# Kernel optimization log

Measured on AMD Instinct MI355X. Metric: run time of the kernel, lower is better.

## Reference

```python
import jax, jax.numpy as jnp
import numpy as np

T = 2048        # Tmax encoder frames
EPROJS = 1024   # encoder projection dim (Henc)
DUNITS = 512    # prediction net hidden
EMBED = 512     # embedding dim
JOINT = 512     # joint space dim
ODIM = 10000    # output vocab
BLANK = 0


def setup_inputs() -> dict:
    key = jax.random.key(0)
    ks = jax.random.split(key, 11)
    def g(k, shape, scale):
        return (jax.random.normal(k, shape, dtype=jnp.float32) * scale)
    inp = {
        'h': jax.random.normal(ks[0], (T, EPROJS), dtype=jnp.float32),
        # Embedding with padding_idx=blank -> blank row zeroed
        'embed': g(ks[1], (ODIM, EMBED), 0.05).at[BLANK].set(0.0),
        # LSTMCell params (torch gate order: i, f, g, o)
        'W_ih': g(ks[2], (4 * DUNITS, EMBED), 1.0 / np.sqrt(EMBED)),
        'W_hh': g(ks[3], (4 * DUNITS, DUNITS), 1.0 / np.sqrt(DUNITS)),
        'b_ih': g(ks[4], (4 * DUNITS,), 0.01),
        'b_hh': g(ks[5], (4 * DUNITS,), 0.01),
        # joint network
        'W_enc': g(ks[6], (JOINT, EPROJS), 1.0 / np.sqrt(EPROJS)),
        'b_enc': g(ks[7], (JOINT,), 0.01),
        'W_dec': g(ks[8], (JOINT, DUNITS), 1.0 / np.sqrt(DUNITS)),  # no bias
        'W_out': g(ks[9], (ODIM, JOINT), 1.0 / np.sqrt(JOINT)),
        'b_out': g(ks[10], (ODIM,), 0.01),
    }
    return inp


def _lstm_cell(x, h_prev, c_prev, W_ih, W_hh, b_ih, b_hh):
    gates = W_ih @ x + b_ih + W_hh @ h_prev + b_hh  # (4*DUNITS,)
    i, f, g, o = jnp.split(gates, 4)
    c = jax.nn.sigmoid(f) * c_prev + jax.nn.sigmoid(i) * jnp.tanh(g)
    h = jax.nn.sigmoid(o) * jnp.tanh(c)
    return h, c


def reference(h, embed, W_ih, W_hh, b_ih, b_hh, W_enc, b_enc, W_dec, W_out, b_out):
    # Precompute encoder-side joint projection (same math, hoisted out of loop)
    h_proj = h @ W_enc.T + b_enc  # (T, JOINT)

    # Initial prediction-net step on zero embedding from zero state
    zeros_e = jnp.zeros((EMBED,), dtype=h.dtype)
    zeros_d = jnp.zeros((DUNITS,), dtype=h.dtype)
    y0, c0 = _lstm_cell(zeros_e, zeros_d, zeros_d, W_ih, W_hh, b_ih, b_hh)

    def step(carry, hp_t):
        y, c, score = carry
        # joint: tanh(lin_enc(h_t) + lin_dec(y)) -> lin_out -> log_softmax
        ytu = jax.nn.log_softmax(W_out @ jnp.tanh(hp_t + W_dec @ y) + b_out)
        logp = jnp.max(ytu)
        pred = jnp.argmax(ytu)
        emitted = pred != BLANK
        # Candidate prediction-net update with embedded token
        ey = embed[pred]
        y_new, c_new = _lstm_cell(ey, y, c, W_ih, W_hh, b_ih, b_hh)
        y = jnp.where(emitted, y_new, y)
        c = jnp.where(emitted, c_new, c)
        score = score + jnp.where(emitted, logp, jnp.zeros_like(logp))
        tok = jnp.where(emitted, pred, BLANK).astype(jnp.int32)
        return (y, c, score), tok

    (y, c, score), yseq = jax.lax.scan(step, (y0, c0, jnp.float32(0.0)), h_proj)
    # yseq: (T,) int32, BLANK where no symbol was emitted at that frame
    return yseq, score
```

## Files before the change

kernel.cpp:

```cpp
#include <hip/hip_runtime.h>
#include <stdint.h>

typedef unsigned long long u64;
typedef uint32_t u32;

#define NB     256
#define NT     256
#define TMAX   2048
#define EPROJS 1024
#define DUNITS 512
#define EMBED  512
#define JOINT  512
#define ODIM   10000

#define N_LSTM 32
#define DEC0   32
#define CONS0  48
#define N_CONS 208
#define MAGIC  0xD07ED07Eu

#define WS_YB   0
#define WS_UD   4096
#define WS_PK   8192
#define WS_SA   10240
#define WS_DN   12288
#define WS_HP   16384

__device__ __forceinline__ float aloadf(const float* p){
  return __hip_atomic_load(p, __ATOMIC_RELAXED, __HIP_MEMORY_SCOPE_AGENT);
}
__device__ __forceinline__ void astoref(float* p, float v){
  __hip_atomic_store(p, v, __ATOMIC_RELAXED, __HIP_MEMORY_SCOPE_AGENT);
}
__device__ __forceinline__ u64 aloadu64(const u64* p){
  return __hip_atomic_load(p, __ATOMIC_RELAXED, __HIP_MEMORY_SCOPE_AGENT);
}
__device__ __forceinline__ void astoreu64(u64* p, u64 v){
  __hip_atomic_store(p, v, __ATOMIC_RELAXED, __HIP_MEMORY_SCOPE_AGENT);
}
__device__ __forceinline__ u32 aloadu32(const u32* p){
  return __hip_atomic_load(p, __ATOMIC_RELAXED, __HIP_MEMORY_SCOPE_AGENT);
}
__device__ __forceinline__ void astoreu32(u32* p, u32 v){
  __hip_atomic_store(p, v, __ATOMIC_RELAXED, __HIP_MEMORY_SCOPE_AGENT);
}

__device__ __forceinline__ u32 ordbits(float f){
  u32 u = __float_as_uint(f);
  return (u & 0x80000000u) ? ~u : (u | 0x80000000u);
}
__device__ __forceinline__ float unordbits(u32 o){
  u32 u = (o & 0x80000000u) ? (o & 0x7fffffffu) : ~o;
  return __uint_as_float(u);
}
__device__ __forceinline__ float sigmoidf_(float x){ return 1.0f/(1.0f+expf(-x)); }

__device__ __forceinline__ float wredsum(float v){
  #pragma unroll
  for (int o=32;o>0;o>>=1) v += __shfl_xor(v, o);
  return v;
}
__device__ __forceinline__ u64 wredmax64(u64 v){
  #pragma unroll
  for (int o=32;o>0;o>>=1){ u64 x = __shfl_xor(v, o); v = (x>v)?x:v; }
  return v;
}

#define LOAD8(dst, baseptr) { const float4* _p=(const float4*)(baseptr); \
  float4 _a=_p[0], _b=_p[1]; \
  dst[0]=_a.x; dst[1]=_a.y; dst[2]=_a.z; dst[3]=_a.w; \
  dst[4]=_b.x; dst[5]=_b.y; dst[6]=_b.z; dst[7]=_b.w; }

#define LDS8(dst, base) { float4 _a=*(const float4*)(base); \
  float4 _b=*(const float4*)((base)+4); \
  dst[0]=_a.x; dst[1]=_a.y; dst[2]=_a.z; dst[3]=_a.w; \
  dst[4]=_b.x; dst[5]=_b.y; dst[6]=_b.z; dst[7]=_b.w; }

__global__ void rnnt_init(char* ws){
  u32* p = (u32*)ws;
  for (int i = threadIdx.x; i < 4096; i += blockDim.x) p[i] = 0u;
}

__global__ void __launch_bounds__(NT, 1)
rnnt_decode(const float* __restrict__ h,    const float* __restrict__ embed,
            const float* __restrict__ W_ih, const float* __restrict__ W_hh,
            const float* __restrict__ b_ih, const float* __restrict__ b_hh,
            const float* __restrict__ W_enc,const float* __restrict__ b_enc,
            const float* __restrict__ W_dec,const float* __restrict__ W_out,
            const float* __restrict__ b_out,
            float* __restrict__ out, char* __restrict__ ws)
{
  const int b    = blockIdx.x;
  const int tid  = threadIdx.x;
  const int lane = tid & 63;
  const int w    = tid >> 6;

  u64*   ybuf = (u64*)(ws + WS_YB);
  u64*   udec = (u64*)(ws + WS_UD);
  u64*   packs= (u64*)(ws + WS_PK);
  u64*   sarr = (u64*)(ws + WS_SA);
  u32*   done = (u32*)(ws + WS_DN);
  float* hp   = (float*)(ws + WS_HP);

  __shared__ float smem[8192];
  float* PL = smem;
  float* EL = &smem[4416];
  float* YL = &smem[4928];
  float* ZL = &smem[5440];
  float* GL = &smem[5952];
  u64*   R64= (u64*)&smem[6016];
  float* RF = &smem[6024];

  {
    float (*lds_h)[EPROJS] = (float(*)[EPROJS])smem;
    #pragma unroll
    for (int r=0;r<8;r++){
      const float4 hv = *(const float4*)(h + (size_t)(8*b + r)*EPROJS + tid*4);
      *(float4*)&lds_h[r][tid*4] = hv;
    }
    __syncthreads();
    for (int p=0;p<2;p++){
      const int j = p*NT + tid;
      float acc[8] = {0,0,0,0,0,0,0,0};
      const float4* wrow = (const float4*)(W_enc + (size_t)j*EPROJS);
      for (int k4=0;k4<EPROJS/4;k4++){
        const float4 wv = wrow[k4];
        #pragma unroll
        for (int t8=0;t8<8;t8++){
          const float4 hv = *(const float4*)&lds_h[t8][k4*4];
          acc[t8] = fmaf(wv.x,hv.x, fmaf(wv.y,hv.y, fmaf(wv.z,hv.z, fmaf(wv.w,hv.w, acc[t8]))));
        }
      }
      const float be = b_enc[j];
      #pragma unroll
      for (int t8=0;t8<8;t8++)
        astoref(&hp[(size_t)(8*b+t8)*JOINT + j], acc[t8] + be);
    }
    asm volatile("s_waitcnt vmcnt(0)" ::: "memory");
    if (tid==0) astoreu32(&done[b], MAGIC);
    __syncthreads();
  }

  if (b < N_LSTM){
    const int d = b;
    float wih[16][8], whh[16][8];
    #pragma unroll
    for (int q=0;q<16;q++){
      const int gr = w*DUNITS + 16*d + q;
      LOAD8(wih[q], W_ih + (size_t)gr*EMBED  + lane*8);
      LOAD8(whh[q], W_hh + (size_t)gr*DUNITS + lane*8);
    }
    float bias_r = 0.0f;
    if (tid < 64){
      const int gr = (tid>>4)*DUNITS + 16*d + (tid&15);
      bias_r = b_ih[gr] + b_hh[gr];
    }
    float c_st = 0.0f, y_st = 0.0f;
    if (tid < 16){
      const int j = 16*d + tid;
      const float gi = b_ih[j]            + b_hh[j];
      const float gg = b_ih[2*DUNITS + j] + b_hh[2*DUNITS + j];
      const float go = b_ih[3*DUNITS + j] + b_hh[3*DUNITS + j];
      c_st = sigmoidf_(gi)*tanhf(gg);
      y_st = sigmoidf_(go)*tanhf(c_st);
      astoreu64(&ybuf[j], ((u64)1u<<32) | (u64)__float_as_uint(y_st));
    }

    for (int t=0;t<TMAX;t++){
      const u32 tg = (u32)(t+1);
      u64 ya, yb;
      for(;;){
        ya = aloadu64(&ybuf[2*tid]); yb = aloadu64(&ybuf[2*tid+1]);
        const int ok = ((u32)(ya>>32)==tg) & ((u32)(yb>>32)==tg);
        if (__syncthreads_and(ok)) break;
      }
      YL[2*tid]   = __uint_as_float((u32)ya);
      YL[2*tid+1] = __uint_as_float((u32)yb);
      __syncthreads();
      float y8[8]; LDS8(y8, &YL[8*lane]);
      float vp[16];
      #pragma unroll
      for (int q=0;q<16;q++){
        float a=0.f;
        #pragma unroll
        for (int k=0;k<8;k++) a = fmaf(whh[q][k], y8[k], a);
        vp[q] = a;
      }
      u64 pk = 0;
      for(;;){
        if (tid < N_CONS) pk = aloadu64(&packs[tid]);
        const int ok = (tid < N_CONS) ? ((u32)(pk>>48)==tg) : 1;
        if (__syncthreads_and(ok)) break;
      }
      { u64 m = wredmax64(pk); if (lane==0) R64[w]=m; }
      __syncthreads();
      if (tid==0){
        u64 bb=R64[0];
        #pragma unroll
        for (int i=1;i<4;i++) bb = (R64[i]>bb)?R64[i]:bb;
        R64[0]=bb;
      }
      __syncthreads();
      const u64 best = R64[0];
      const int pred = (int)((~(u32)best) & 0xFFFFu);
      const int emitted = (pred != 0);
      __syncthreads();
      const float2 ev = *(const float2*)(embed + (size_t)pred*EMBED + 2*tid);
      EL[2*tid] = ev.x; EL[2*tid+1] = ev.y;
      __syncthreads();
      float e8[8]; LDS8(e8, &EL[8*lane]);
      #pragma unroll
      for (int q=0;q<16;q++){
        float a = vp[q];
        #pragma unroll
        for (int k=0;k<8;k++) a = fmaf(wih[q][k], e8[k], a);
        PL[(w*16+q)*68 + lane] = a;
      }
      __syncthreads();
      if (tid < 64){
        const float* row = &PL[tid*68];
        float s = bias_r;
        #pragma unroll
        for (int k4=0;k4<16;k4++){
          const float4 v4 = *(const float4*)&row[4*k4];
          s += v4.x + v4.y + v4.z + v4.w;
        }
        GL[tid] = s;
      }
      __syncthreads();
      if (tid < 16){
        const float gi=GL[tid], gf=GL[16+tid], gg=GL[32+tid], go=GL[48+tid];
        const float cn = sigmoidf_(gf)*c_st + sigmoidf_(gi)*tanhf(gg);
        const float yn = sigmoidf_(go)*tanhf(cn);
        if (emitted){ c_st = cn; y_st = yn; }
        astoreu64(&ybuf[16*d + tid], ((u64)(tg+1)<<32) | (u64)__float_as_uint(y_st));
      }
    }
  }
  else if (b < CONS0){
    const int dd = b - DEC0;
    float wdec[8][8];
    #pragma unroll
    for (int q=0;q<8;q++){
      const int r = 32*dd + 8*w + q;
      LOAD8(wdec[q], W_dec + (size_t)r*DUNITS + lane*8);
    }
    for (int t=0;t<TMAX;t++){
      const u32 tg = (u32)(t+1);
      u64 ya, yb;
      for(;;){
        ya = aloadu64(&ybuf[2*tid]); yb = aloadu64(&ybuf[2*tid+1]);
        const int ok = ((u32)(ya>>32)==tg) & ((u32)(yb>>32)==tg);
        if (__syncthreads_and(ok)) break;
      }
      YL[2*tid]   = __uint_as_float((u32)ya);
      YL[2*tid+1] = __uint_as_float((u32)yb);
      __syncthreads();
      float y8[8]; LDS8(y8, &YL[8*lane]);
      #pragma unroll
      for (int q=0;q<8;q++){
        float a=0.f;
        #pragma unroll
        for (int k=0;k<8;k++) a = fmaf(wdec[q][k], y8[k], a);
        PL[(8*w+q)*68 + lane] = a;
      }
      __syncthreads();
      if (tid < 32){
        const float* row = &PL[tid*68];
        float s = 0.f;
        #pragma unroll
        for (int k4=0;k4<16;k4++){
          const float4 v4 = *(const float4*)&row[4*k4];
          s += v4.x + v4.y + v4.z + v4.w;
        }
        astoreu64(&udec[32*dd + tid], ((u64)tg<<32) | (u64)__float_as_uint(s));
      }
      __syncthreads();
    }
  }
  else {
    const int cb = b - CONS0;
    const int rowstart = (cb<16) ? cb*49 : 784 + (cb-16)*48;
    const int rowcnt   = (cb<16) ? 49 : 48;
    float wout[13][8];
    #pragma unroll
    for (int q=0;q<13;q++){
      const int s = 13*w + q;
      if (s < rowcnt){
        LOAD8(wout[q], W_out + (size_t)(rowstart+s)*JOINT + lane*8);
      } else {
        #pragma unroll
        for (int k=0;k<8;k++) wout[q][k]=0.f;
      }
    }
    float my_bo = 0.f; int my_row = 0; bool my_val = false;
    if (tid < rowcnt){ my_val = true; my_row = rowstart + tid; my_bo = b_out[my_row]; }

    for(;;){
      const int ok = (aloadu32(&done[tid]) == MAGIC);
      if (__syncthreads_and(ok)) break;
    }

    float score = 0.0f;
    for (int t=0;t<TMAX;t++){
      const u32 tg = (u32)(t+1);
      u64 ua, ub;
      for(;;){
        ua = aloadu64(&udec[2*tid]); ub = aloadu64(&udec[2*tid+1]);
        const int ok = ((u32)(ua>>32)==tg) & ((u32)(ub>>32)==tg);
        if (__syncthreads_and(ok)) break;
      }
      const float u0 = __uint_as_float((u32)ua);
      const float u1 = __uint_as_float((u32)ub);
      const float h0 = aloadf(&hp[(size_t)t*JOINT + 2*tid]);
      const float h1 = aloadf(&hp[(size_t)t*JOINT + 2*tid + 1]);
      ZL[2*tid]   = tanhf(h0 + u0);
      ZL[2*tid+1] = tanhf(h1 + u1);
      __syncthreads();
      float z8[8]; LDS8(z8, &ZL[8*lane]);
      #pragma unroll
      for (int q=0;q<13;q++){
        float a=0.f;
        #pragma unroll
        for (int k=0;k<8;k++) a = fmaf(wout[q][k], z8[k], a);
        PL[(13*w+q)*68 + lane] = a;
      }
      __syncthreads();
      u64 key = 0; float lg = 0.f;
      if (tid < 52){
        const float* row = &PL[tid*68];
        float s = my_bo;
        #pragma unroll
        for (int k4=0;k4<16;k4++){
          const float4 v4 = *(const float4*)&row[4*k4];
          s += v4.x + v4.y + v4.z + v4.w;
        }
        lg = s;
        if (my_val) key = ((u64)ordbits(lg)<<16) | (u64)(0xFFFFu & ~(u32)my_row);
      }
      if (w == 0){
        const u64 bk = wredmax64(key);
        const float mw = unordbits((u32)(bk>>16));
        const float e  = my_val ? __expf(lg - mw) : 0.f;
        const float sw = wredsum(e);
        if (lane == 0){
          astoreu64(&sarr[cb],  ((u64)tg<<32) | (u64)__float_as_uint(sw));
          astoreu64(&packs[cb], ((u64)tg<<48) | bk);
        }
      }
      if (b == CONS0){
        u64 pk = 0, sa = 0;
        for(;;){
          if (tid < N_CONS){ pk = aloadu64(&packs[tid]); sa = aloadu64(&sarr[tid]); }
          const int ok = (tid < N_CONS) ?
            (((u32)(pk>>48)==tg) & ((u32)(sa>>32)==tg)) : 1;
          if (__syncthreads_and(ok)) break;
        }
        { u64 m = wredmax64(pk); if (lane==0) R64[w]=m; }
        __syncthreads();
        if (tid==0){
          u64 bb=R64[0];
          #pragma unroll
          for (int i=1;i<4;i++) bb = (R64[i]>bb)?R64[i]:bb;
          R64[0]=bb;
        }
        __syncthreads();
        const u64 best = R64[0];
        const float mstar = unordbits((u32)(best>>16));
        float term = (tid < N_CONS) ?
          __uint_as_float((u32)sa) * __expf(unordbits((u32)(pk>>16)) - mstar) : 0.f;
        term = wredsum(term);
        if (lane==0) RF[w]=term;
        __syncthreads();
        if (tid==0){
          const float S = RF[0]+RF[1]+RF[2]+RF[3];
          const int pred = (int)((~(u32)best) & 0xFFFFu);
          if (pred != 0) score += -logf(S);
          out[t] = (float)pred;
        }
        __syncthreads();
      } else {
        __syncthreads();
      }
    }
    if (b == CONS0 && tid == 0) out[TMAX] = score;
  }
}

extern "C" void kernel_launch(void* const* d_in, const int* in_sizes, int n_in,
                              void* d_out, int out_size, void* d_ws, size_t ws_size,
                              hipStream_t stream)
{
  const float* h     = (const float*)d_in[0];
  const float* embed = (const float*)d_in[1];
  const float* W_ih  = (const float*)d_in[2];
  const float* W_hh  = (const float*)d_in[3];
  const float* b_ih  = (const float*)d_in[4];
  const float* b_hh  = (const float*)d_in[5];
  const float* W_enc = (const float*)d_in[6];
  const float* b_enc = (const float*)d_in[7];
  const float* W_dec = (const float*)d_in[8];
  const float* W_out = (const float*)d_in[9];
  const float* b_out = (const float*)d_in[10];
  float* out = (float*)d_out;
  char* ws = (char*)d_ws;

  hipLaunchKernelGGL(rnnt_init, dim3(1), dim3(NT), 0, stream, ws);
  hipLaunchKernelGGL(rnnt_decode, dim3(NB), dim3(NT), 0, stream,
                     h, embed, W_ih, W_hh, b_ih, b_hh, W_enc, b_enc, W_dec, W_out, b_out,
                     out, ws);
}
```

Before: 18.24 ms.

## Fold decoder projection into LSTM blocks and use counter-based sync with ring buffers

Removes the separate W_dec blocks. Each LSTM block now computes its partial W_dec·y contribution and atomically accumulates it into a double-buffered u vector. A counter signals readiness, replacing the per-element tagged-flag polling. Pack/sum slots become a 4-deep ring, the final aggregation moves to a dedicated block, and more blocks act as consumers, each handling fewer output rows. This shortens the critical path per timestep and reduces polling traffic, at the cost of float atomicAdd nondeterminism and more subtle buffer-reuse ordering.

```diff
diff --git a/kernel.cpp b/kernel.cpp
--- a/kernel.cpp
+++ b/kernel.cpp
@@ -14,17 +14,18 @@
 #define ODIM   10000
 
 #define N_LSTM 32
-#define DEC0   32
-#define CONS0  48
-#define N_CONS 208
+#define CONS0  32
+#define N_CONS 223
+#define AGG_B  255
 #define MAGIC  0xD07ED07Eu
 
-#define WS_YB   0
-#define WS_UD   4096
+#define WS_Y    0
+#define WS_U    4096
 #define WS_PK   8192
-#define WS_SA   10240
-#define WS_DN   12288
-#define WS_HP   16384
+#define WS_SA   15360
+#define WS_DN   22528
+#define WS_CNT  23552
+#define WS_HP   32768
 
 __device__ __forceinline__ float aloadf(const float* p){
   return __hip_atomic_load(p, __ATOMIC_RELAXED, __HIP_MEMORY_SCOPE_AGENT);
@@ -78,7 +79,7 @@
 
 __global__ void rnnt_init(char* ws){
   u32* p = (u32*)ws;
-  for (int i = threadIdx.x; i < 4096; i += blockDim.x) p[i] = 0u;
+  for (int i = threadIdx.x; i < 8192; i += blockDim.x) p[i] = 0u;
 }
 
 __global__ void __launch_bounds__(NT, 1)
@@ -95,11 +96,12 @@
   const int lane = tid & 63;
   const int w    = tid >> 6;
 
-  u64*   ybuf = (u64*)(ws + WS_YB);
-  u64*   udec = (u64*)(ws + WS_UD);
-  u64*   packs= (u64*)(ws + WS_PK);
-  u64*   sarr = (u64*)(ws + WS_SA);
-  u32*   done = (u32*)(ws + WS_DN);
+  float* ybuf = (float*)(ws + WS_Y);
+  float* ubuf = (float*)(ws + WS_U);
+  u64*  pkall = (u64*)(ws + WS_PK);
+  u64*  saall = (u64*)(ws + WS_SA);
+  u32*  done  = (u32*)(ws + WS_DN);
+  u32*  cnt   = (u32*)(ws + WS_CNT);
   float* hp   = (float*)(ws + WS_HP);
 
   __shared__ float smem[8192];
@@ -110,6 +112,7 @@
   float* GL = &smem[5952];
   u64*   R64= (u64*)&smem[6016];
   float* RF = &smem[6024];
+  float* YO = &smem[6032];
 
   {
     float (*lds_h)[EPROJS] = (float(*)[EPROJS])smem;
@@ -150,6 +153,18 @@
       LOAD8(wih[q], W_ih + (size_t)gr*EMBED  + lane*8);
       LOAD8(whh[q], W_hh + (size_t)gr*DUNITS + lane*8);
     }
+    float wdc0[16], wdc1[16];
+    {
+      const float4* p0 = (const float4*)(W_dec + (size_t)(2*tid)*DUNITS   + 16*d);
+      const float4* p1 = (const float4*)(W_dec + (size_t)(2*tid+1)*DUNITS + 16*d);
+      #pragma unroll
+      for (int k4=0;k4<4;k4++){
+        const float4 a = p0[k4];
+        wdc0[4*k4+0]=a.x; wdc0[4*k4+1]=a.y; wdc0[4*k4+2]=a.z; wdc0[4*k4+3]=a.w;
+        const float4 c = p1[k4];
+        wdc1[4*k4+0]=c.x; wdc1[4*k4+1]=c.y; wdc1[4*k4+2]=c.z; wdc1[4*k4+3]=c.w;
+      }
+    }
     float bias_r = 0.0f;
     if (tid < 64){
       const int gr = (tid>>4)*DUNITS + 16*d + (tid&15);
@@ -163,19 +178,31 @@
       const float go = b_ih[3*DUNITS + j] + b_hh[3*DUNITS + j];
       c_st = sigmoidf_(gi)*tanhf(gg);
       y_st = sigmoidf_(go)*tanhf(c_st);
-      astoreu64(&ybuf[j], ((u64)1u<<32) | (u64)__float_as_uint(y_st));
-    }
+      YO[tid] = y_st;
+      astoref(&ybuf[512 + j], y_st);
+    }
+    __syncthreads();
+    {
+      float p0=0.f, p1=0.f;
+      #pragma unroll
+      for (int k=0;k<16;k++){ p0 = fmaf(wdc0[k], YO[k], p0); p1 = fmaf(wdc1[k], YO[k], p1); }
+      atomicAdd(&ubuf[512 + 2*tid],   p0);
+      atomicAdd(&ubuf[512 + 2*tid+1], p1);
+    }
+    asm volatile("s_waitcnt vmcnt(0)" ::: "memory");
+    __syncthreads();
+    if (tid < 8) atomicAdd(&cnt[tid*32], 1u);
 
     for (int t=0;t<TMAX;t++){
-      const u32 tg = (u32)(t+1);
-      u64 ya, yb;
-      for(;;){
-        ya = aloadu64(&ybuf[2*tid]); yb = aloadu64(&ybuf[2*tid+1]);
-        const int ok = ((u32)(ya>>32)==tg) & ((u32)(yb>>32)==tg);
-        if (__syncthreads_and(ok)) break;
-      }
-      YL[2*tid]   = __uint_as_float((u32)ya);
-      YL[2*tid+1] = __uint_as_float((u32)yb);
+      const u32 g = (u32)(t+1);
+      if (tid==0){ while (aloadu32(&cnt[(d&7)*32]) < 32u*g) {} }
+      __syncthreads();
+      {
+        const u64* y64 = (const u64*)(ws + WS_Y + (g&1)*2048);
+        const u64 v = aloadu64(&y64[tid]);
+        YL[2*tid]   = __uint_as_float((u32)v);
+        YL[2*tid+1] = __uint_as_float((u32)(v>>32));
+      }
       __syncthreads();
       float y8[8]; LDS8(y8, &YL[8*lane]);
       float vp[16];
@@ -187,26 +214,26 @@
         vp[q] = a;
       }
       u64 pk = 0;
-      for(;;){
-        if (tid < N_CONS) pk = aloadu64(&packs[tid]);
-        const int ok = (tid < N_CONS) ? ((u32)(pk>>48)==tg) : 1;
-        if (__syncthreads_and(ok)) break;
+      {
+        const u64* pks = pkall + (g&3)*224;
+        for(;;){
+          pk = (tid < N_CONS) ? aloadu64(&pks[tid]) : 0;
+          const int ok = (tid < N_CONS) ? ((u32)(pk>>48) >= g) : 1;
+          if (__all(ok)) break;
+        }
       }
       { u64 m = wredmax64(pk); if (lane==0) R64[w]=m; }
       __syncthreads();
-      if (tid==0){
-        u64 bb=R64[0];
-        #pragma unroll
-        for (int i=1;i<4;i++) bb = (R64[i]>bb)?R64[i]:bb;
-        R64[0]=bb;
-      }
-      __syncthreads();
-      const u64 best = R64[0];
+      u64 best = R64[0];
+      #pragma unroll
+      for (int i=1;i<4;i++){ const u64 x=R64[i]; best = (x>best)?x:best; }
       const int pred = (int)((~(u32)best) & 0xFFFFu);
       const int emitted = (pred != 0);
-      __syncthreads();
-      const float2 ev = *(const float2*)(embed + (size_t)pred*EMBED + 2*tid);
-      EL[2*tid] = ev.x; EL[2*tid+1] = ev.y;
+      if (tid < 16) astoref(&ubuf[(g&1)*512 + 16*d + tid], 0.0f);
+      {
+        const float2 ev = *(const float2*)(embed + (size_t)pred*EMBED + 2*tid);
+        EL[2*tid] = ev.x; EL[2*tid+1] = ev.y;
+      }
       __syncthreads();
       float e8[8]; LDS8(e8, &EL[8*lane]);
       #pragma unroll
@@ -233,59 +260,32 @@
         const float cn = sigmoidf_(gf)*c_st + sigmoidf_(gi)*tanhf(gg);
         const float yn = sigmoidf_(go)*tanhf(cn);
         if (emitted){ c_st = cn; y_st = yn; }
-        astoreu64(&ybuf[16*d + tid], ((u64)(tg+1)<<32) | (u64)__float_as_uint(y_st));
-      }
+        YO[tid] = y_st;
+        astoref(&ybuf[((g+1)&1)*512 + 16*d + tid], y_st);
+      }
+      __syncthreads();
+      if (t < TMAX-1){
+        float p0=0.f, p1=0.f;
+        #pragma unroll
+        for (int k=0;k<16;k++){ p0 = fmaf(wdc0[k], YO[k], p0); p1 = fmaf(wdc1[k], YO[k], p1); }
+        float* up = &ubuf[((g+1)&1)*512];
+        atomicAdd(&up[2*tid],   p0);
+        atomicAdd(&up[2*tid+1], p1);
+      }
+      asm volatile("s_waitcnt vmcnt(0)" ::: "memory");
+      __syncthreads();
+      if (t < TMAX-1 && tid < 8) atomicAdd(&cnt[tid*32], 1u);
     }
   }
-  else if (b < CONS0){
-    const int dd = b - DEC0;
-    float wdec[8][8];
+  else if (b < AGG_B){
+    const int cb = b - CONS0;
+    int rowstart, rowcnt;
+    if (cb < 188){ rowstart = cb*45;                 rowcnt = 45; }
+    else         { rowstart = 8460 + (cb-188)*44;    rowcnt = 44; }
+    float wout[12][8];
     #pragma unroll
-    for (int q=0;q<8;q++){
-      const int r = 32*dd + 8*w + q;
-      LOAD8(wdec[q], W_dec + (size_t)r*DUNITS + lane*8);
-    }
-    for (int t=0;t<TMAX;t++){
-      const u32 tg = (u32)(t+1);
-      u64 ya, yb;
-      for(;;){
-        ya = aloadu64(&ybuf[2*tid]); yb = aloadu64(&ybuf[2*tid+1]);
-        const int ok = ((u32)(ya>>32)==tg) & ((u32)(yb>>32)==tg);
-        if (__syncthreads_and(ok)) break;
-      }
-      YL[2*tid]   = __uint_as_float((u32)ya);
-      YL[2*tid+1] = __uint_as_float((u32)yb);
-      __syncthreads();
-      float y8[8]; LDS8(y8, &YL[8*lane]);
-      #pragma unroll
-      for (int q=0;q<8;q++){
-        float a=0.f;
-        #pragma unroll
-        for (int k=0;k<8;k++) a = fmaf(wdec[q][k], y8[k], a);
-        PL[(8*w+q)*68 + lane] = a;
-      }
-      __syncthreads();
-      if (tid < 32){
-        const float* row = &PL[tid*68];
-        float s = 0.f;
-        #pragma unroll
-        for (int k4=0;k4<16;k4++){
-          const float4 v4 = *(const float4*)&row[4*k4];
-          s += v4.x + v4.y + v4.z + v4.w;
-        }
-        astoreu64(&udec[32*dd + tid], ((u64)tg<<32) | (u64)__float_as_uint(s));
-      }
-      __syncthreads();
-    }
-  }
-  else {
-    const int cb = b - CONS0;
-    const int rowstart = (cb<16) ? cb*49 : 784 + (cb-16)*48;
-    const int rowcnt   = (cb<16) ? 49 : 48;
-    float wout[13][8];
-    #pragma unroll
-    for (int q=0;q<13;q++){
-      const int s = 13*w + q;
+    for (int q=0;q<12;q++){
+      const int s = 12*w + q;
       if (s < rowcnt){
         LOAD8(wout[q], W_out + (size_t)(rowstart+s)*JOINT + lane*8);
       } else {
@@ -297,37 +297,35 @@
     if (tid < rowcnt){ my_val = true; my_row = rowstart + tid; my_bo = b_out[my_row]; }
 
     for(;;){
-      const int ok = (aloadu32(&done[tid]) == MAGIC);
-      if (__syncthreads_and(ok)) break;
-    }
-
-    float score = 0.0f;
+      const u32 dv = aloadu32(&done[tid]);
+      if (__all(dv == MAGIC)) break;
+    }
+    __syncthreads();
+
+    const u32* cp = &cnt[(cb&7)*32];
     for (int t=0;t<TMAX;t++){
-      const u32 tg = (u32)(t+1);
-      u64 ua, ub;
-      for(;;){
-        ua = aloadu64(&udec[2*tid]); ub = aloadu64(&udec[2*tid+1]);
-        const int ok = ((u32)(ua>>32)==tg) & ((u32)(ub>>32)==tg);
-        if (__syncthreads_and(ok)) break;
-      }
-      const float u0 = __uint_as_float((u32)ua);
-      const float u1 = __uint_as_float((u32)ub);
+      const u32 g = (u32)(t+1);
       const float h0 = aloadf(&hp[(size_t)t*JOINT + 2*tid]);
       const float h1 = aloadf(&hp[(size_t)t*JOINT + 2*tid + 1]);
+      if (tid==0){ while (aloadu32(cp) < 32u*g) {} }
+      __syncthreads();
+      const u64 uv = aloadu64(&((const u64*)(ws + WS_U + (g&1)*2048))[tid]);
+      const float u0 = __uint_as_float((u32)uv);
+      const float u1 = __uint_as_float((u32)(uv>>32));
       ZL[2*tid]   = tanhf(h0 + u0);
       ZL[2*tid+1] = tanhf(h1 + u1);
       __syncthreads();
       float z8[8]; LDS8(z8, &ZL[8*lane]);
       #pragma unroll
-      for (int q=0;q<13;q++){
+      for (int q=0;q<12;q++){
         float a=0.f;
         #pragma unroll
         for (int k=0;k<8;k++) a = fmaf(wout[q][k], z8[k], a);
-        PL[(13*w+q)*68 + lane] = a;
+        PL[(12*w+q)*68 + lane] = a;
       }
       __syncthreads();
       u64 key = 0; float lg = 0.f;
-      if (tid < 52){
+      if (tid < 48){
         const float* row = &PL[tid*68];
         float s = my_bo;
         #pragma unroll
@@ -344,46 +342,44 @@
         const float e  = my_val ? __expf(lg - mw) : 0.f;
         const float sw = wredsum(e);
         if (lane == 0){
-          astoreu64(&sarr[cb],  ((u64)tg<<32) | (u64)__float_as_uint(sw));
-          astoreu64(&packs[cb], ((u64)tg<<48) | bk);
+          astoreu64(&saall[(g&3)*224 + cb], ((u64)g<<32) | (u64)__float_as_uint(sw));
+          astoreu64(&pkall[(g&3)*224 + cb], ((u64)g<<48) | bk);
         }
       }
-      if (b == CONS0){
-        u64 pk = 0, sa = 0;
-        for(;;){
-          if (tid < N_CONS){ pk = aloadu64(&packs[tid]); sa = aloadu64(&sarr[tid]); }
-          const int ok = (tid < N_CONS) ?
-            (((u32)(pk>>48)==tg) & ((u32)(sa>>32)==tg)) : 1;
-          if (__syncthreads_and(ok)) break;
-        }
-        { u64 m = wredmax64(pk); if (lane==0) R64[w]=m; }
-        __syncthreads();
-        if (tid==0){
-          u64 bb=R64[0];
-          #pragma unroll
-          for (int i=1;i<4;i++) bb = (R64[i]>bb)?R64[i]:bb;
-          R64[0]=bb;
-        }
-        __syncthreads();
-        const u64 best = R64[0];
-        const float mstar = unordbits((u32)(best>>16));
-        float term = (tid < N_CONS) ?
-          __uint_as_float((u32)sa) * __expf(unordbits((u32)(pk>>16)) - mstar) : 0.f;
-        term = wredsum(term);
-        if (lane==0) RF[w]=term;
-        __syncthreads();
-        if (tid==0){
-          const float S = RF[0]+RF[1]+RF[2]+RF[3];
-          const int pred = (int)((~(u32)best) & 0xFFFFu);
-          if (pred != 0) score += -logf(S);
-          out[t] = (float)pred;
-        }
-        __syncthreads();
-      } else {
-        __syncthreads();
-      }
-    }
-    if (b == CONS0 && tid == 0) out[TMAX] = score;
+    }
+  }
+  else {
+    float score = 0.0f;
+    for (int t=0;t<TMAX;t++){
+      const u32 g = (u32)(t+1);
+      const u64* pks = pkall + (g&3)*224;
+      const u64* sas = saall + (g&3)*224;
+      u64 pk=0, sa=0;
+      for(;;){
+        if (tid < N_CONS){ pk = aloadu64(&pks[tid]); sa = aloadu64(&sas[tid]); }
+        const int ok = (tid < N_CONS) ? (((u32)(pk>>48) >= g) & ((u32)(sa>>32) >= g)) : 1;
+        if (__all(ok)) break;
+      }
+      { u64 m = wredmax64(pk); if (lane==0) R64[w]=m; }
+      __syncthreads();
+      u64 best = R64[0];
+      #pragma unroll
+      for (int i=1;i<4;i++){ const u64 x=R64[i]; best = (x>best)?x:best; }
+      const float mstar = unordbits((u32)(best>>16));
+      float term = (tid < N_CONS) ?
+        __uint_as_float((u32)sa) * __expf(unordbits((u32)(pk>>16)) - mstar) : 0.f;
+      term = wredsum(term);
+      if (lane==0) RF[w] = term;
+      __syncthreads();
+      if (tid==0){
+        const float S = RF[0]+RF[1]+RF[2]+RF[3];
+        const int pred = (int)((~(u32)best) & 0xFFFFu);
+        if (pred != 0) score += -logf(S);
+        out[t] = (float)pred;
+      }
+      __syncthreads();
+    }
+    if (tid==0) out[TMAX] = score;
   }
 }
 
```

Result: faster. 16.98 ms (-6.9%).
